# Kernel tuning notes

Measured on AMD Instinct MI355X. Metric: run time of the kernel, lower is better.

Reference implementation:

```python
import jax, jax.numpy as jnp
import numpy as np

B, P, ENC = 128, 625, 512
A, E, H, V = 256, 256, 512, 70
START_TOK, END_TOK = 68, 69


def setup_inputs() -> dict:
    key = jax.random.key(0)
    ks = jax.random.split(key, 20)
    w = lambda k, shape: jax.random.normal(k, shape, jnp.float32) * 0.02
    return {
        "encoder_out": jax.random.normal(ks[0], (B, P, ENC), jnp.float32),
        "emb": w(ks[1], (V, E)),
        "We": w(ks[2], (ENC, A)), "be": jnp.zeros((A,), jnp.float32),
        "Wd": w(ks[3], (H, A)),   "bd": jnp.zeros((A,), jnp.float32),
        "wf": w(ks[4], (A,)),     "bf": jnp.zeros((), jnp.float32),
        "Wh0": w(ks[5], (ENC, H)), "bh0": jnp.zeros((H,), jnp.float32),
        "Wc0": w(ks[6], (ENC, H)), "bc0": jnp.zeros((H,), jnp.float32),
        "Wb": w(ks[7], (H, ENC)), "bb": jnp.zeros((ENC,), jnp.float32),
        "Wih": w(ks[8], (E + ENC, 4 * H)), "Whh": w(ks[9], (H, 4 * H)),
        "bih": jnp.zeros((4 * H,), jnp.float32), "bhh": jnp.zeros((4 * H,), jnp.float32),
        "Wfc": w(ks[10], (H, V)), "bfc": jnp.zeros((V,), jnp.float32),
        "decode_lengths": 70,
    }


def _decode(encoder_out, emb, We, be, Wd, bd, wf, bf, Wh0, bh0, Wc0, bc0,
            Wb, bb, Wih, Whh, bih, bhh, Wfc, bfc, decode_lengths):
    enc = encoder_out  # [B, P, ENC]
    batch = enc.shape[0]
    # encoder_att projection is constant across timesteps -> hoist out of loop
    att1 = enc @ We + be                      # [B, P, A]
    mean_enc = enc.mean(axis=1)               # [B, ENC]
    h0 = mean_enc @ Wh0 + bh0                 # [B, H]
    c0 = mean_enc @ Wc0 + bc0                 # [B, H]
    emb0 = emb[jnp.full((batch,), START_TOK)]  # [B, E]
    lstm_b = bih + bhh

    def step(carry, _):
        h, c, emb_t, done = carry
        att2 = h @ Wd + bd                                            # [B, A]
        e = jnp.einsum('bpa,a->bp', jax.nn.relu(att1 + att2[:, None, :]), wf) + bf
        alpha = jax.nn.softmax(e, axis=1)                             # [B, P]
        awe = jnp.einsum('bp,bpe->be', alpha, enc)                    # [B, ENC]
        awe = jax.nn.sigmoid(h @ Wb + bb) * awe                       # gated
        gates = jnp.concatenate([emb_t, awe], axis=1) @ Wih + h @ Whh + lstm_b
        i_, f_, g_, o_ = jnp.split(gates, 4, axis=1)                  # torch order i,f,g,o
        c_new = jax.nn.sigmoid(f_) * c + jax.nn.sigmoid(i_) * jnp.tanh(g_)
        h_new = jax.nn.sigmoid(o_) * jnp.tanh(c_new)
        preds = h_new @ Wfc + bfc                                     # [B, V] (dropout eval = id)
        preds_out = jnp.where(done, 0.0, preds)                       # zeros after early break
        done_new = done | (jnp.argmax(preds) == END_TOK)              # flat argmax, as in torch
        emb_new = emb[jnp.argmax(preds, axis=-1)]                     # greedy feedback
        return (h_new, c_new, emb_new, done_new), preds_out

    init = (h0, c0, emb0, jnp.array(False))
    _, preds_seq = jax.lax.scan(step, init, None, length=decode_lengths)
    return jnp.transpose(preds_seq, (1, 0, 2))  # [B, T, V]


def reference(encoder_out, emb, We, be, Wd, bd, wf, bf, Wh0, bh0, Wc0, bc0,
              Wb, bb, Wih, Whh, bih, bhh, Wfc, bfc, decode_lengths):
    return _decode(encoder_out, emb, We, be, Wd, bd, wf, bf, Wh0, bh0, Wc0, bc0,
                   Wb, bb, Wih, Whh, bih, bhh, Wfc, bfc, decode_lengths)
```

## Files before the change

kernel.cpp:

```cpp
#include <hip/hip_runtime.h>
#include <math.h>

#define Bn 128
#define Pn 625
#define ENCn 512
#define An 256
#define En 256
#define Hn 512
#define Vn 70
#define G4n 2048
#define STARTT 68
#define ENDT 69
#define NCHUNK 5
#define PCH 125
#define PSTRIDE 520
#define KSPLIT 16
#define KCH 80


__global__ __launch_bounds__(256) void k_mean(const float* __restrict__ enc,
                                              float* __restrict__ mean_enc) {
  int b = blockIdx.x, t = threadIdx.x;
  const float* e = enc + (size_t)b * Pn * ENCn;
  float s0 = 0.f, s1 = 0.f;
  for (int p = 0; p < Pn; ++p) {
    s0 += e[(size_t)p * ENCn + t];
    s1 += e[(size_t)p * ENCn + t + 256];
  }
  mean_enc[b * ENCn + t] = s0 * (1.0f / 625.0f);
  mean_enc[b * ENCn + t + 256] = s1 * (1.0f / 625.0f);
}

__global__ __launch_bounds__(256) void k_prep(const float* __restrict__ Wfc,
                                              float* __restrict__ WfcT) {
  int j = blockIdx.x * 256 + threadIdx.x;
  if (j < Hn * Vn) {
    int k = j / Vn, vv = j - k * Vn;
    WfcT[(size_t)vv * Hn + k] = Wfc[j];
  }
}

__global__ __launch_bounds__(512) void k_init(const float* __restrict__ mean_enc,
                       const float* __restrict__ Wh0, const float* __restrict__ bh0,
                       const float* __restrict__ Wc0, const float* __restrict__ bc0,
                       const float* __restrict__ emb,
                       float* __restrict__ h0, float* __restrict__ c0,
                       float* __restrict__ emb_t, int* __restrict__ done_arr) {
  int b = blockIdx.x, t = threadIdx.x;
  const float* W = blockIdx.y ? Wc0 : Wh0;
  const float* bias = blockIdx.y ? bc0 : bh0;
  float* out = blockIdx.y ? c0 : h0;
  __shared__ float ms[ENCn];
  ms[t] = mean_enc[b * ENCn + t];
  __syncthreads();
  float s = bias[t];
  for (int k = 0; k < ENCn; ++k) s += ms[k] * W[k * Hn + t];
  out[b * Hn + t] = s;
  if (blockIdx.y == 0 && t < En) emb_t[b * En + t] = emb[STARTT * En + t];
  if (blockIdx.y == 0 && b == 0 && t == 0) done_arr[0] = 0;
}

__global__ __launch_bounds__(256) void k_att1(const float* __restrict__ Am,
                       const float* __restrict__ We,
                       const float* __restrict__ be, float* __restrict__ att1) {
  __shared__ float sA[16][128];
  __shared__ float sB[16][128];
  int n0 = blockIdx.x * 128, m0 = blockIdx.y * 128;
  int t = threadIdx.x;
  int tm = (t >> 4) * 8, tn = (t & 15) * 8;
  float acc[8][8];
#pragma unroll
  for (int i = 0; i < 8; ++i)
#pragma unroll
    for (int j = 0; j < 8; ++j) acc[i][j] = 0.f;
  for (int k0 = 0; k0 < 512; k0 += 16) {
    __syncthreads();
#pragma unroll
    for (int i = 0; i < 8; ++i) {
      int idx = t + i * 256;
      int mm = idx >> 4, kk = idx & 15;
      sA[kk][mm] = Am[(size_t)(m0 + mm) * 512 + k0 + kk];
      int kk2 = idx >> 7, nn = idx & 127;
      sB[kk2][nn] = We[(size_t)(k0 + kk2) * 256 + n0 + nn];
    }
    __syncthreads();
#pragma unroll
    for (int kk = 0; kk < 16; ++kk) {
      float a[8], bq[8];
      *(float4*)&a[0] = *(const float4*)&sA[kk][tm];
      *(float4*)&a[4] = *(const float4*)&sA[kk][tm + 4];
      *(float4*)&bq[0] = *(const float4*)&sB[kk][tn];
      *(float4*)&bq[4] = *(const float4*)&sB[kk][tn + 4];
#pragma unroll
      for (int i = 0; i < 8; ++i)
#pragma unroll
        for (int j = 0; j < 8; ++j) acc[i][j] += a[i] * bq[j];
    }
  }
  float ber[8];
  *(float4*)&ber[0] = *(const float4*)&be[n0 + tn];
  *(float4*)&ber[4] = *(const float4*)&be[n0 + tn + 4];
#pragma unroll
  for (int i = 0; i < 8; ++i) {
    float o[8];
#pragma unroll
    for (int j = 0; j < 8; ++j) o[j] = acc[i][j] + ber[j];
    *(float4*)&att1[(size_t)(m0 + tm + i) * An + n0 + tn] = *(float4*)&o[0];
    *(float4*)&att1[(size_t)(m0 + tm + i) * An + n0 + tn + 4] = *(float4*)&o[4];
  }
}


__global__ __launch_bounds__(256) void k_proj(const float* __restrict__ h,
                       const float* __restrict__ Wd, const float* __restrict__ bd,
                       const float* __restrict__ Wb, const float* __restrict__ bbv,
                       float* __restrict__ att2, float* __restrict__ gate,
                       const float* __restrict__ preds,
                       const int* __restrict__ done_prev, int* __restrict__ done_cur,
                       int do_flat) {
  int t = threadIdx.x;
  if (blockIdx.x == Bn) {
    if (!do_flat) return;
    __shared__ float sv[256];
    __shared__ int si[256];
    float bv = -1e30f; int bi = 0x7fffffff;
    for (int i = t; i < Bn * Vn; i += 256) {
      float v = preds[i];
      if (v > bv) { bv = v; bi = i; }
    }
    sv[t] = bv; si[t] = bi;
    __syncthreads();
    for (int s = 128; s > 0; s >>= 1) {
      if (t < s) {
        if (sv[t + s] > sv[t] || (sv[t + s] == sv[t] && si[t + s] < si[t])) {
          sv[t] = sv[t + s]; si[t] = si[t + s];
        }
      }
      __syncthreads();
    }
    if (t == 0) *done_cur = (*done_prev) | (si[0] == ENDT ? 1 : 0);
    return;
  }
  int b = blockIdx.x;
  __shared__ float hsh[Hn];
  hsh[t] = h[b * Hn + t];
  hsh[t + 256] = h[b * Hn + t + 256];
  __syncthreads();
  float s0 = bd[t];
  float s1 = bbv[t], s2 = bbv[t + 256];
  for (int k = 0; k < Hn; ++k) {
    float hv = hsh[k];
    s0 += hv * Wd[(size_t)k * An + t];
    s1 += hv * Wb[(size_t)k * ENCn + t];
    s2 += hv * Wb[(size_t)k * ENCn + t + 256];
  }
  att2[b * An + t] = s0;
  gate[b * ENCn + t] = 1.f / (1.f + expf(-s1));
  gate[b * ENCn + t + 256] = 1.f / (1.f + expf(-s2));
}

__global__ __launch_bounds__(256) void k_attn(const float* __restrict__ att1,
                       const float* __restrict__ att2,
                       const float* __restrict__ wf, const float* __restrict__ bfp,
                       const float* __restrict__ enc, float* __restrict__ part) {
  int c = blockIdx.x, b = blockIdx.y, t = threadIdx.x;
  int lane = t & 63, wv = t >> 6;
  int p0 = c * PCH;
  __shared__ float es[PCH];
  __shared__ float red[256];
  float4 a2 = ((const float4*)(att2 + b * An))[lane];
  float4 wfr = ((const float4*)wf)[lane];
  float bfv = *bfp;
  const float* a1b = att1 + ((size_t)b * Pn + p0) * An;
  for (int p = wv; p < PCH; p += 4) {
    float4 v = ((const float4*)(a1b + (size_t)p * An))[lane];
    float s = fmaxf(v.x + a2.x, 0.f) * wfr.x
            + fmaxf(v.y + a2.y, 0.f) * wfr.y
            + fmaxf(v.z + a2.z, 0.f) * wfr.z
            + fmaxf(v.w + a2.w, 0.f) * wfr.w;
    for (int o = 32; o > 0; o >>= 1) s += __shfl_down(s, o, 64);
    if (lane == 0) es[p] = s + bfv;
  }
  __syncthreads();
  float m = -1e30f;
  for (int i = t; i < PCH; i += 256) m = fmaxf(m, es[i]);
  red[t] = m;
  __syncthreads();
  for (int s = 128; s > 0; s >>= 1) {
    if (t < s) red[t] = fmaxf(red[t], red[t + s]);
    __syncthreads();
  }
  m = red[0];
  __syncthreads();
  float lp = 0.f;
  for (int i = t; i < PCH; i += 256) {
    float e2 = expf(es[i] - m);
    es[i] = e2;
    lp += e2;
  }
  red[t] = lp;
  __syncthreads();
  for (int s = 128; s > 0; s >>= 1) {
    if (t < s) red[t] += red[t + s];
    __syncthreads();
  }
  float l = red[0];
  float acc0 = 0.f, acc1 = 0.f;
  const float* ebase = enc + ((size_t)b * Pn + p0) * ENCn;
  int p = 0;
#pragma unroll 4
  for (; p + 1 < PCH; p += 2) {
    float wp0 = es[p], wp1 = es[p + 1];
    float2 ev0 = ((const float2*)(ebase + (size_t)p * ENCn))[t];
    float2 ev1 = ((const float2*)(ebase + (size_t)(p + 1) * ENCn))[t];
    acc0 += wp0 * ev0.x;
    acc1 += wp0 * ev0.y;
    acc0 += wp1 * ev1.x;
    acc1 += wp1 * ev1.y;
  }
  if (p < PCH) {
    float wp = es[p];
    float2 ev = ((const float2*)(ebase + (size_t)p * ENCn))[t];
    acc0 += wp * ev.x;
    acc1 += wp * ev.y;
  }
  float* pp = part + (size_t)(b * NCHUNK + c) * PSTRIDE;
  if (t == 0) { pp[0] = m; pp[1] = l; }
  *(float2*)&pp[8 + 2 * t] = make_float2(acc0, acc1);
}

__global__ __launch_bounds__(256) void k_combine(const float* __restrict__ part,
                       const float* __restrict__ gate, float* __restrict__ awe) {
  int b = blockIdx.x, t = threadIdx.x;
  const float* pb = part + (size_t)b * NCHUNK * PSTRIDE;
  float M = -1e30f;
#pragma unroll
  for (int c = 0; c < NCHUNK; ++c) M = fmaxf(M, pb[c * PSTRIDE]);
  float L = 0.f, sc[NCHUNK];
#pragma unroll
  for (int c = 0; c < NCHUNK; ++c) {
    float s = expf(pb[c * PSTRIDE] - M);
    sc[c] = s;
    L += s * pb[c * PSTRIDE + 1];
  }
  float inv = 1.f / L;
  float a0 = 0.f, a1 = 0.f;
#pragma unroll
  for (int c = 0; c < NCHUNK; ++c) {
    a0 += sc[c] * pb[c * PSTRIDE + 8 + t];
    a1 += sc[c] * pb[c * PSTRIDE + 8 + t + 256];
  }
  awe[b * ENCn + t] = a0 * inv * gate[b * ENCn + t];
  awe[b * ENCn + t + 256] = a1 * inv * gate[b * ENCn + t + 256];
}

__global__ __launch_bounds__(256) void k_gates(const float* __restrict__ embt,
                       const float* __restrict__ awe, const float* __restrict__ h,
                       const float* __restrict__ Wih, const float* __restrict__ Whh,
                       float* __restrict__ gp) {
  int n0 = blockIdx.x * 64;
  int sI = blockIdx.y;
  int k0 = sI * KCH;
  int t = threadIdx.x;
  int tc = t & 15, tg = t >> 4;
  int nc = n0 + tc * 4;
  float4 acc[8];
#pragma unroll
  for (int r = 0; r < 8; ++r) acc[r] = make_float4(0.f, 0.f, 0.f, 0.f);
  for (int kk = 0; kk < KCH; kk += 4) {
    int k = k0 + kk;
    const float* wbase = (k < 768) ? (Wih + (size_t)k * G4n + nc)
                                   : (Whh + (size_t)(k - 768) * G4n + nc);
    float4 w0 = *(const float4*)(wbase);
    float4 w1 = *(const float4*)(wbase + G4n);
    float4 w2 = *(const float4*)(wbase + 2 * G4n);
    float4 w3 = *(const float4*)(wbase + 3 * G4n);
#pragma unroll
    for (int r = 0; r < 8; ++r) {
      int row = tg * 8 + r;
      float4 xv;
      if (k < 256)      xv = *(const float4*)(embt + row * En + k);
      else if (k < 768) xv = *(const float4*)(awe + row * ENCn + (k - 256));
      else              xv = *(const float4*)(h + row * Hn + (k - 768));
      acc[r].x += xv.x * w0.x + xv.y * w1.x + xv.z * w2.x + xv.w * w3.x;
      acc[r].y += xv.x * w0.y + xv.y * w1.y + xv.z * w2.y + xv.w * w3.y;
      acc[r].z += xv.x * w0.z + xv.y * w1.z + xv.z * w2.z + xv.w * w3.z;
      acc[r].w += xv.x * w0.w + xv.y * w1.w + xv.z * w2.w + xv.w * w3.w;
    }
  }
#pragma unroll
  for (int r = 0; r < 8; ++r)
    *(float4*)(gp + ((size_t)sI * Bn + tg * 8 + r) * G4n + nc) = acc[r];
}

__global__ __launch_bounds__(512) void k_lstm(const float* __restrict__ gp,
                       const float* __restrict__ bih, const float* __restrict__ bhh,
                       const float* __restrict__ c_in, float* __restrict__ c_out,
                       float* __restrict__ h_out,
                       const float* __restrict__ WfcT, const float* __restrict__ bfc,
                       const float* __restrict__ emb, float* __restrict__ preds,
                       float* __restrict__ emb_next, float* __restrict__ out,
                       const int* __restrict__ done_t, int step, int T) {
  int b = blockIdx.x, t = threadIdx.x;
  float gi = bih[t] + bhh[t];
  float gf = bih[t + 512] + bhh[t + 512];
  float gg = bih[t + 1024] + bhh[t + 1024];
  float go = bih[t + 1536] + bhh[t + 1536];
  for (int s = 0; s < KSPLIT; ++s) {
    const float* row = gp + ((size_t)s * Bn + b) * G4n;
    gi += row[t];
    gf += row[t + 512];
    gg += row[t + 1024];
    go += row[t + 1536];
  }
  float cv = (1.f / (1.f + expf(-gf))) * c_in[b * Hn + t]
           + (1.f / (1.f + expf(-gi))) * tanhf(gg);
  float hv = (1.f / (1.f + expf(-go))) * tanhf(cv);
  c_out[b * Hn + t] = cv;
  h_out[b * Hn + t] = hv;
  __shared__ float hs[Hn];
  __shared__ float ps[Vn];
  __shared__ int tokS;
  hs[t] = hv;
  __syncthreads();
  int lane = t & 63, wvi = t >> 6;
  for (int v = wvi; v < Vn; v += 8) {
    float s = 0.f;
    for (int k = lane; k < Hn; k += 64) s += hs[k] * WfcT[(size_t)v * Hn + k];
    for (int o = 32; o > 0; o >>= 1) s += __shfl_down(s, o, 64);
    if (lane == 0) ps[v] = s + bfc[v];
  }
  __syncthreads();
  int done = *done_t;
  if (t < Vn) {
    float pv = ps[t];
    preds[b * Vn + t] = pv;
    out[((size_t)b * T + step) * Vn + t] = done ? 0.f : pv;
  }
  if (t == 0) {
    float bv = ps[0]; int bi = 0;
    for (int v = 1; v < Vn; ++v)
      if (ps[v] > bv) { bv = ps[v]; bi = v; }
    tokS = bi;
  }
  __syncthreads();
  if (t < En) emb_next[b * En + t] = emb[tokS * En + t];
}


extern "C" void kernel_launch(void* const* d_in, const int* in_sizes, int n_in,
                              void* d_out, int out_size, void* d_ws, size_t ws_size,
                              hipStream_t stream) {
  const float* enc = (const float*)d_in[0];
  const float* emb = (const float*)d_in[1];
  const float* We  = (const float*)d_in[2];
  const float* be  = (const float*)d_in[3];
  const float* Wd  = (const float*)d_in[4];
  const float* bd  = (const float*)d_in[5];
  const float* wf  = (const float*)d_in[6];
  const float* bf  = (const float*)d_in[7];
  const float* Wh0 = (const float*)d_in[8];
  const float* bh0 = (const float*)d_in[9];
  const float* Wc0 = (const float*)d_in[10];
  const float* bc0 = (const float*)d_in[11];
  const float* Wb  = (const float*)d_in[12];
  const float* bb  = (const float*)d_in[13];
  const float* Wih = (const float*)d_in[14];
  const float* Whh = (const float*)d_in[15];
  const float* bih = (const float*)d_in[16];
  const float* bhh = (const float*)d_in[17];
  const float* Wfc = (const float*)d_in[18];
  const float* bfc = (const float*)d_in[19];
  int T = out_size / (Bn * Vn);

  float* w = (float*)d_ws;
  size_t off = 0;
  float* att1 = w + off;     off += (size_t)Bn * Pn * An;
  float* WfcT = w + off;     off += (size_t)Hn * Vn;
  float* mean_enc = w + off; off += Bn * ENCn;
  float* hb0 = w + off;      off += Bn * Hn;
  float* hb1 = w + off;      off += Bn * Hn;
  float* cb0 = w + off;      off += Bn * Hn;
  float* cb1 = w + off;      off += Bn * Hn;
  float* eb0 = w + off;      off += Bn * En;
  float* eb1 = w + off;      off += Bn * En;
  float* att2 = w + off;     off += Bn * An;
  float* gate = w + off;     off += Bn * ENCn;
  float* part = w + off;     off += (size_t)Bn * NCHUNK * PSTRIDE;
  float* awe = w + off;      off += Bn * ENCn;
  float* gatesP = w + off;   off += (size_t)KSPLIT * Bn * G4n;
  float* preds = w + off;    off += Bn * Vn;
  off = (off + 255) & ~(size_t)255;
  int* done_arr = (int*)(w + off);

  float* hbuf[2] = {hb0, hb1};
  float* cbuf[2] = {cb0, cb1};
  float* ebuf[2] = {eb0, eb1};

  k_mean<<<Bn, 256, 0, stream>>>(enc, mean_enc);
  k_prep<<<(Hn * Vn + 255) / 256, 256, 0, stream>>>(Wfc, WfcT);
  k_init<<<dim3(Bn, 2), 512, 0, stream>>>(mean_enc, Wh0, bh0, Wc0, bc0, emb,
                                          hb0, cb0, eb0, done_arr);
  k_att1<<<dim3(2, 625), 256, 0, stream>>>(enc, We, be, att1);

  int cur = 0;
  for (int t = 0; t < T; ++t) {
    int nxt = cur ^ 1;
    k_proj<<<Bn + 1, 256, 0, stream>>>(hbuf[cur], Wd, bd, Wb, bb, att2, gate, preds,
                                       done_arr + (t > 0 ? t - 1 : 0), done_arr + t,
                                       t > 0 ? 1 : 0);
    k_attn<<<dim3(NCHUNK, Bn), 256, 0, stream>>>(att1, att2, wf, bf, enc, part);
    k_combine<<<Bn, 256, 0, stream>>>(part, gate, awe);
    k_gates<<<dim3(32, KSPLIT), 256, 0, stream>>>(ebuf[cur], awe, hbuf[cur], Wih, Whh, gatesP);
    k_lstm<<<Bn, 512, 0, stream>>>(gatesP, bih, bhh, cbuf[cur], cbuf[nxt], hbuf[nxt],
                                   WfcT, bfc, emb, preds, ebuf[nxt], (float*)d_out,
                                   done_arr + t, t, T);
    cur = nxt;
  }
}
```

Before: 9.157 ms.

## Vectorize att1 tile loads, split mean kernel grid, add unroll pragmas

k_att1 now fills its shared tiles with float4 global loads instead of scalar loads. k_mean is split across two blocks per batch row, doubling its parallelism. Unroll pragmas are added to the loops in k_init, k_proj, k_attn and k_lstm. These target load-instruction overhead and latency in one-off and per-step kernels, at the cost of possible transposed shared-store bank conflicts in sA and higher register pressure.

```diff
diff --git a/kernel.cpp b/kernel.cpp
--- a/kernel.cpp
+++ b/kernel.cpp
@@ -20,15 +20,12 @@
 
 __global__ __launch_bounds__(256) void k_mean(const float* __restrict__ enc,
                                               float* __restrict__ mean_enc) {
-  int b = blockIdx.x, t = threadIdx.x;
-  const float* e = enc + (size_t)b * Pn * ENCn;
-  float s0 = 0.f, s1 = 0.f;
-  for (int p = 0; p < Pn; ++p) {
-    s0 += e[(size_t)p * ENCn + t];
-    s1 += e[(size_t)p * ENCn + t + 256];
-  }
-  mean_enc[b * ENCn + t] = s0 * (1.0f / 625.0f);
-  mean_enc[b * ENCn + t + 256] = s1 * (1.0f / 625.0f);
+  int b = blockIdx.x, col = blockIdx.y * 256 + threadIdx.x;
+  const float* e = enc + (size_t)b * Pn * ENCn + col;
+  float s = 0.f;
+#pragma unroll 4
+  for (int p = 0; p < Pn; ++p) s += e[(size_t)p * ENCn];
+  mean_enc[b * ENCn + col] = s * (1.0f / 625.0f);
 }
 
 __global__ __launch_bounds__(256) void k_prep(const float* __restrict__ Wfc,
@@ -54,6 +51,7 @@
   ms[t] = mean_enc[b * ENCn + t];
   __syncthreads();
   float s = bias[t];
+#pragma unroll 8
   for (int k = 0; k < ENCn; ++k) s += ms[k] * W[k * Hn + t];
   out[b * Hn + t] = s;
   if (blockIdx.y == 0 && t < En) emb_t[b * En + t] = emb[STARTT * En + t];
@@ -68,6 +66,8 @@
   int n0 = blockIdx.x * 128, m0 = blockIdx.y * 128;
   int t = threadIdx.x;
   int tm = (t >> 4) * 8, tn = (t & 15) * 8;
+  int a_row = t >> 1, a_k = (t & 1) * 8;
+  int b_kk = t >> 4, b_nn = (t & 15) * 8;
   float acc[8][8];
 #pragma unroll
   for (int i = 0; i < 8; ++i)
@@ -75,13 +75,17 @@
     for (int j = 0; j < 8; ++j) acc[i][j] = 0.f;
   for (int k0 = 0; k0 < 512; k0 += 16) {
     __syncthreads();
-#pragma unroll
-    for (int i = 0; i < 8; ++i) {
-      int idx = t + i * 256;
-      int mm = idx >> 4, kk = idx & 15;
-      sA[kk][mm] = Am[(size_t)(m0 + mm) * 512 + k0 + kk];
-      int kk2 = idx >> 7, nn = idx & 127;
-      sB[kk2][nn] = We[(size_t)(k0 + kk2) * 256 + n0 + nn];
+    {
+      const float* ap = Am + (size_t)(m0 + a_row) * 512 + k0 + a_k;
+      float4 a0 = *(const float4*)ap;
+      float4 a1 = *(const float4*)(ap + 4);
+      sA[a_k + 0][a_row] = a0.x; sA[a_k + 1][a_row] = a0.y;
+      sA[a_k + 2][a_row] = a0.z; sA[a_k + 3][a_row] = a0.w;
+      sA[a_k + 4][a_row] = a1.x; sA[a_k + 5][a_row] = a1.y;
+      sA[a_k + 6][a_row] = a1.z; sA[a_k + 7][a_row] = a1.w;
+      const float* bp = We + (size_t)(k0 + b_kk) * 256 + n0 + b_nn;
+      *(float4*)&sB[b_kk][b_nn] = *(const float4*)bp;
+      *(float4*)&sB[b_kk][b_nn + 4] = *(const float4*)(bp + 4);
     }
     __syncthreads();
 #pragma unroll
@@ -148,6 +152,7 @@
   __syncthreads();
   float s0 = bd[t];
   float s1 = bbv[t], s2 = bbv[t + 256];
+#pragma unroll 8
   for (int k = 0; k < Hn; ++k) {
     float hv = hsh[k];
     s0 += hv * Wd[(size_t)k * An + t];
@@ -172,6 +177,7 @@
   float4 wfr = ((const float4*)wf)[lane];
   float bfv = *bfp;
   const float* a1b = att1 + ((size_t)b * Pn + p0) * An;
+#pragma unroll 2
   for (int p = wv; p < PCH; p += 4) {
     float4 v = ((const float4*)(a1b + (size_t)p * An))[lane];
     float s = fmaxf(v.x + a2.x, 0.f) * wfr.x
@@ -306,6 +312,7 @@
   float gf = bih[t + 512] + bhh[t + 512];
   float gg = bih[t + 1024] + bhh[t + 1024];
   float go = bih[t + 1536] + bhh[t + 1536];
+#pragma unroll 4
   for (int s = 0; s < KSPLIT; ++s) {
     const float* row = gp + ((size_t)s * Bn + b) * G4n;
     gi += row[t];
@@ -326,6 +333,7 @@
   int lane = t & 63, wvi = t >> 6;
   for (int v = wvi; v < Vn; v += 8) {
     float s = 0.f;
+#pragma unroll
     for (int k = lane; k < Hn; k += 64) s += hs[k] * WfcT[(size_t)v * Hn + k];
     for (int o = 32; o > 0; o >>= 1) s += __shfl_down(s, o, 64);
     if (lane == 0) ps[v] = s + bfc[v];
@@ -397,7 +405,7 @@
   float* cbuf[2] = {cb0, cb1};
   float* ebuf[2] = {eb0, eb1};
 
-  k_mean<<<Bn, 256, 0, stream>>>(enc, mean_enc);
+  k_mean<<<dim3(Bn, 2), 256, 0, stream>>>(enc, mean_enc);
   k_prep<<<(Hn * Vn + 255) / 256, 256, 0, stream>>>(Wfc, WfcT);
   k_init<<<dim3(Bn, 2), 512, 0, stream>>>(mean_enc, Wh0, bh0, Wc0, bc0, emb,
                                           hb0, cb0, eb0, done_arr);
```

New measurement: 9.242 ms. No clear change (+0.9%).
